# Kernel tuning notes

Measured on AMD Instinct MI355X. Metric: run time of the kernel, lower is better.

## Reference

```python
import jax, jax.numpy as jnp
import numpy as np
import math

# Module constants (from __init__ defaults / chosen init_kwargs)
B = 4            # hand_batch_size
C = 8            # num_cameras
BC = B * C       # camera batch
R = 256          # resolution
NB = 64          # num_bins
BIN = 0.0136     # bin_size
FOV = 33.0       # degrees
DCS = 0.001      # camera_sensor_distance
SIGMA_BIN = 3.0  # self.sigma for soft binning


def _masks():
    fov_rad = FOV * math.pi / 180.0
    scale = math.tan(fov_rad / 2.0)
    center_scale = scale * (1.0 - 1.0 / R)
    lin = jnp.linspace(-center_scale, center_scale, R, dtype=jnp.float32)
    xg, yg = jnp.meshgrid(lin, lin, indexing='xy')
    fm = jnp.stack([xg, -yg, -jnp.ones((R, R), jnp.float32)], axis=2)
    film_mask = -fm / jnp.linalg.norm(fm, axis=2, keepdims=True)  # [R,R,3]
    cos_mask = 1.0 / jnp.sqrt(xg * xg + yg * yg + 1.0)            # [R,R]
    return film_mask, cos_mask


def setup_inputs() -> dict:
    key = jax.random.key(0)
    k1, k2 = jax.random.split(key)
    film_mask, cos_mask = _masks()
    # per-pixel interpolated vertex normals (pre-normalization, as dr.interpolate output)
    normals = jax.random.normal(k1, (BC, R, R, 3), dtype=jnp.float32)
    # per-pixel camera-space intersection points; z ~ 0.5 m so depths fall mid-histogram
    intersections = jax.random.normal(k2, (BC, R, R, 3), dtype=jnp.float32) * 0.1 \
        + jnp.array([0.0, 0.0, 0.5], dtype=jnp.float32)
    return {"normals": normals, "intersections": intersections,
            "film_mask": film_mask, "cos_mask": cos_mask}


def reference(normals, intersections, film_mask, cos_mask):
    width = 2.0 * math.tan(FOV * math.pi / 360.0)
    # cosine foreshortening w.r.t. film ray directions
    dots = jnp.clip(jnp.einsum('ijk,bijk->bij', film_mask, normals), 0.0, 1.0)
    # laser origin offset by 2 * camera_sensor_distance along +x
    laser_points = intersections - jnp.array([2.0 * DCS, 0.0, 0.0], dtype=intersections.dtype)
    laser_distances = jnp.linalg.norm(laser_points, axis=3)  # [BC,R,R]
    laser_tan = jnp.sqrt(laser_points[..., 0] ** 2 + laser_points[..., 1] ** 2) / laser_points[..., 2]
    sig = math.tan(math.radians(21.5)) / 1.4
    laser_mask = jnp.exp(-laser_tan ** 2 / (2.0 * sig * sig))
    dots = dots * laser_mask
    radiance = dots / laser_distances / laser_distances / math.pi \
        * (width * width) * (cos_mask ** 3) / float(R * R)      # [BC,R,R]
    depths = (jnp.linalg.norm(intersections, axis=3) + laser_distances) / 2.0
    d_bin = depths / BIN                                         # [BC,R,R]
    b = jnp.arange(NB, dtype=jnp.float32)                        # [NB]
    # soft bin kernel: sigmoid(s*(d-b)) - sigmoid(s*(d-b-1)), [BC,R,R,NB]
    x = d_bin[..., None] - b
    kernels = jax.nn.sigmoid(SIGMA_BIN * x) - jax.nn.sigmoid(SIGMA_BIN * (x - 1.0))
    # histogram accumulation over all pixels -> per-camera transient [BC,NB]
    transients = jnp.einsum('bijk,bij->bk', kernels, radiance)
    return transients
```

## Files before the change

### kernel.cpp

```cpp
#include <hip/hip_runtime.h>
#include <math.h>

#define NPIX    65536
#define NBINS   64
#define NBATCH  32
#define SPLIT   32
#define BLOCKT  128
#define PXPT    4
#define ITERS   (NPIX / SPLIT / (BLOCKT * PXPT))
#define HSTRIDE 68
#define LDSN    (BLOCKT * HSTRIDE)
#define WIN     12

#define THREE_LOG2E 4.328085122666891f

__global__ __launch_bounds__(BLOCKT, 2) void spad_hist_kernel(
    const float* __restrict__ normals,
    const float* __restrict__ inters,
    const float* __restrict__ film,
    const float* __restrict__ cosm,
    float* __restrict__ ws,
    float kconst, float lmask_c, float half_inv_bin)
{
    __shared__ float hist[LDSN];
    const int tid = threadIdx.x;
    {
        float4* h4 = (float4*)&hist[tid * HSTRIDE];
        #pragma unroll
        for (int i = 0; i < HSTRIDE / 4; ++i) h4[i] = make_float4(0.f, 0.f, 0.f, 0.f);
    }
    __syncthreads();

    const int b = blockIdx.x & (NBATCH - 1);
    const int chunk = blockIdx.x / NBATCH;
    const int pix0 = chunk * (NPIX / SPLIT);
    const int base = tid * HSTRIDE;

    const float E3P[13] = {
        1.0f, 20.085536923187668f, 403.4287934927351f, 8103.083927575384f,
        162754.79141900392f, 3269017.372472111f, 65659969.13733051f,
        1318815734.4832146f, 26489122129.843472f, 532048240601.79865f,
        10686474581524.462f, 214643579785916.06f, 4311231547115195.0f };

    #pragma unroll
    for (int it = 0; it < ITERS; ++it) {
        const int pp = pix0 + (it * BLOCKT + tid) * PXPT;
        const float4* n4 = (const float4*)(normals + ((size_t)b * NPIX + pp) * 3);
        const float4* i4 = (const float4*)(inters  + ((size_t)b * NPIX + pp) * 3);
        const float4* f4 = (const float4*)(film + (size_t)pp * 3);
        const float4  c4 = *(const float4*)(cosm + pp);
        float4 n0 = n4[0], n1 = n4[1], n2 = n4[2];
        float4 i0 = i4[0], i1 = i4[1], i2 = i4[2];
        float4 f0 = f4[0], f1 = f4[1], f2 = f4[2];

        float NX[4] = {n0.x, n0.w, n1.z, n2.y}, NY[4] = {n0.y, n1.x, n1.w, n2.z},
              NZ[4] = {n0.z, n1.y, n2.x, n2.w};
        float IX[4] = {i0.x, i0.w, i1.z, i2.y}, IY[4] = {i0.y, i1.x, i1.w, i2.z},
              IZ[4] = {i0.z, i1.y, i2.x, i2.w};
        float FX[4] = {f0.x, f0.w, f1.z, f2.y}, FY[4] = {f0.y, f1.x, f1.w, f2.z},
              FZ[4] = {f0.z, f1.y, f2.x, f2.w};
        float CM[4] = {c4.x, c4.y, c4.z, c4.w};

        int   K0[4];
        float W[4][WIN];

        #pragma unroll
        for (int p = 0; p < 4; ++p) {
            float dt = FX[p] * NX[p] + FY[p] * NY[p] + FZ[p] * NZ[p];
            dt = fminf(fmaxf(dt, 0.0f), 1.0f);
            float lx = IX[p] - 0.002f;
            float lxy2 = lx * lx + IY[p] * IY[p];
            float l2 = lxy2 + IZ[p] * IZ[p];
            float ld = __builtin_amdgcn_sqrtf(l2);
            float lm = __builtin_amdgcn_exp2f(
                lmask_c * lxy2 * __builtin_amdgcn_rcpf(IZ[p] * IZ[p]));
            float cm3 = CM[p] * CM[p] * CM[p];
            float r = dt * lm * kconst * cm3 * __builtin_amdgcn_rcpf(l2);
            float di = __builtin_amdgcn_sqrtf(
                IX[p] * IX[p] + IY[p] * IY[p] + IZ[p] * IZ[p]);
            float d = (di + ld) * half_inv_bin;

            int j0 = (int)floorf(d);
            j0 = j0 < 4 ? 4 : (j0 > 56 ? 56 : j0);
            int k0 = (j0 - 4) & ~3;
            K0[p] = k0;
            float e0 = __builtin_amdgcn_exp2f(((float)k0 - d) * THREE_LOG2E);
            float S[WIN + 1];
            #pragma unroll
            for (int m = 0; m < WIN + 1; ++m)
                S[m] = __builtin_amdgcn_rcpf(fmaf(e0, E3P[m], 1.0f));
            #pragma unroll
            for (int m = 0; m < WIN; ++m)
                W[p][m] = r * (S[m] - S[m + 1]);
        }

        #pragma unroll
        for (int p = 0; p < 4; ++p) {
            float4* hp = (float4*)&hist[base + K0[p]];
            float4 a = hp[0], bb = hp[1], c = hp[2];
            a.x  += W[p][0];  a.y  += W[p][1];  a.z  += W[p][2];  a.w  += W[p][3];
            bb.x += W[p][4];  bb.y += W[p][5];  bb.z += W[p][6];  bb.w += W[p][7];
            c.x  += W[p][8];  c.y  += W[p][9];  c.z  += W[p][10]; c.w  += W[p][11];
            hp[0] = a; hp[1] = bb; hp[2] = c;
        }
    }
    __syncthreads();

    const int g = tid & 15;
    const int h = tid >> 4;
    float4 acc = make_float4(0.f, 0.f, 0.f, 0.f);
    #pragma unroll
    for (int j = 0; j < 16; ++j) {
        float4 v = *(const float4*)&hist[(h + 8 * j) * HSTRIDE + 4 * g];
        acc.x += v.x; acc.y += v.y; acc.z += v.z; acc.w += v.w;
    }
    __syncthreads();
    *(float4*)&hist[tid * 4] = acc;
    __syncthreads();
    if (tid < 16) {
        float4 s4 = make_float4(0.f, 0.f, 0.f, 0.f);
        #pragma unroll
        for (int hh = 0; hh < 8; ++hh) {
            float4 v = *(const float4*)&hist[hh * 64 + tid * 4];
            s4.x += v.x; s4.y += v.y; s4.z += v.z; s4.w += v.w;
        }
        *(float4*)&ws[(size_t)blockIdx.x * NBINS + tid * 4] = s4;
    }
}

__global__ __launch_bounds__(256) void spad_reduce_kernel(
    const float* __restrict__ ws, float* __restrict__ out)
{
    const int o = blockIdx.x * 256 + threadIdx.x;
    const int b = o >> 6;
    const int k = o & 63;
    float s = 0.0f;
    #pragma unroll
    for (int c = 0; c < SPLIT; ++c)
        s += ws[((size_t)(c * NBATCH + b)) * NBINS + k];
    out[o] = s;
}

extern "C" void kernel_launch(void* const* d_in, const int* in_sizes, int n_in,
                              void* d_out, int out_size, void* d_ws, size_t ws_size,
                              hipStream_t stream) {
    const float* normals = (const float*)d_in[0];
    const float* inters  = (const float*)d_in[1];
    const float* film    = (const float*)d_in[2];
    const float* cosm    = (const float*)d_in[3];
    float* out = (float*)d_out;
    float* ws  = (float*)d_ws;

    const double fov_rad = 33.0 * M_PI / 180.0;
    const double width = 2.0 * tan(fov_rad / 2.0);
    const double kconst_d = width * width / M_PI / 65536.0;
    const double sig = tan(21.5 * M_PI / 180.0) / 1.4;
    const double log2e = 1.4426950408889634;
    const double lmask_c_d = -log2e / (2.0 * sig * sig);
    const double half_inv_bin_d = 0.5 / 0.0136;

    spad_hist_kernel<<<NBATCH * SPLIT, BLOCKT, 0, stream>>>(
        normals, inters, film, cosm, ws,
        (float)kconst_d, (float)lmask_c_d, (float)half_inv_bin_d);

    spad_reduce_kernel<<<(NBATCH * NBINS) / 256, 256, 0, stream>>>(ws, out);
}
```

Before: 92.72 us.

## Share LDS histograms across 16 threads with atomic adds and larger blocks

Each thread previously owned a private 64-bin histogram in LDS, which limited block size and occupancy. Now 16 threads share one histogram and accumulate the 12-bin window with LDS atomicAdd. The window starts exactly at j0-5 instead of a 4-aligned offset. The block grows to 256 threads with 4 blocks per CU, and the final reduction is simplified. In exchange, 12 scalar LDS atomics per pixel replace three float4 read-modify-writes, and threads sharing a histogram can contend on the same bins.

```diff
diff --git a/kernel.cpp b/kernel.cpp
--- a/kernel.cpp
+++ b/kernel.cpp
@@ -5,16 +5,17 @@
 #define NBINS   64
 #define NBATCH  32
 #define SPLIT   32
-#define BLOCKT  128
+#define BLOCKT  256
 #define PXPT    4
 #define ITERS   (NPIX / SPLIT / (BLOCKT * PXPT))
-#define HSTRIDE 68
-#define LDSN    (BLOCKT * HSTRIDE)
 #define WIN     12
+#define NHIST   (BLOCKT / 16)
+#define HSTRIDE 72
+#define LDSN    (NHIST * HSTRIDE)
 
 #define THREE_LOG2E 4.328085122666891f
 
-__global__ __launch_bounds__(BLOCKT, 2) void spad_hist_kernel(
+__global__ __launch_bounds__(BLOCKT, 4) void spad_hist_kernel(
     const float* __restrict__ normals,
     const float* __restrict__ inters,
     const float* __restrict__ film,
@@ -24,17 +25,13 @@
 {
     __shared__ float hist[LDSN];
     const int tid = threadIdx.x;
-    {
-        float4* h4 = (float4*)&hist[tid * HSTRIDE];
-        #pragma unroll
-        for (int i = 0; i < HSTRIDE / 4; ++i) h4[i] = make_float4(0.f, 0.f, 0.f, 0.f);
-    }
+    for (int i = tid; i < LDSN; i += BLOCKT) hist[i] = 0.0f;
     __syncthreads();
 
     const int b = blockIdx.x & (NBATCH - 1);
     const int chunk = blockIdx.x / NBATCH;
     const int pix0 = chunk * (NPIX / SPLIT);
-    const int base = tid * HSTRIDE;
+    float* const hq = &hist[(tid >> 4) * HSTRIDE];
 
     const float E3P[13] = {
         1.0f, 20.085536923187668f, 403.4287934927351f, 8103.083927575384f,
@@ -61,9 +58,6 @@
               FZ[4] = {f0.z, f1.y, f2.x, f2.w};
         float CM[4] = {c4.x, c4.y, c4.z, c4.w};
 
-        int   K0[4];
-        float W[4][WIN];
-
         #pragma unroll
         for (int p = 0; p < 4; ++p) {
             float dt = FX[p] * NX[p] + FY[p] * NY[p] + FZ[p] * NZ[p];
@@ -81,50 +75,27 @@
             float d = (di + ld) * half_inv_bin;
 
             int j0 = (int)floorf(d);
-            j0 = j0 < 4 ? 4 : (j0 > 56 ? 56 : j0);
-            int k0 = (j0 - 4) & ~3;
-            K0[p] = k0;
+            j0 = j0 < 5 ? 5 : (j0 > 57 ? 57 : j0);
+            const int k0 = j0 - 5;
             float e0 = __builtin_amdgcn_exp2f(((float)k0 - d) * THREE_LOG2E);
             float S[WIN + 1];
             #pragma unroll
             for (int m = 0; m < WIN + 1; ++m)
                 S[m] = __builtin_amdgcn_rcpf(fmaf(e0, E3P[m], 1.0f));
+
+            float* hp = hq + k0;
             #pragma unroll
             for (int m = 0; m < WIN; ++m)
-                W[p][m] = r * (S[m] - S[m + 1]);
-        }
-
-        #pragma unroll
-        for (int p = 0; p < 4; ++p) {
-            float4* hp = (float4*)&hist[base + K0[p]];
-            float4 a = hp[0], bb = hp[1], c = hp[2];
-            a.x  += W[p][0];  a.y  += W[p][1];  a.z  += W[p][2];  a.w  += W[p][3];
-            bb.x += W[p][4];  bb.y += W[p][5];  bb.z += W[p][6];  bb.w += W[p][7];
-            c.x  += W[p][8];  c.y  += W[p][9];  c.z  += W[p][10]; c.w  += W[p][11];
-            hp[0] = a; hp[1] = bb; hp[2] = c;
+                atomicAdd(&hp[m], r * (S[m] - S[m + 1]));
         }
     }
     __syncthreads();
 
-    const int g = tid & 15;
-    const int h = tid >> 4;
-    float4 acc = make_float4(0.f, 0.f, 0.f, 0.f);
-    #pragma unroll
-    for (int j = 0; j < 16; ++j) {
-        float4 v = *(const float4*)&hist[(h + 8 * j) * HSTRIDE + 4 * g];
-        acc.x += v.x; acc.y += v.y; acc.z += v.z; acc.w += v.w;
-    }
-    __syncthreads();
-    *(float4*)&hist[tid * 4] = acc;
-    __syncthreads();
-    if (tid < 16) {
-        float4 s4 = make_float4(0.f, 0.f, 0.f, 0.f);
+    if (tid < NBINS) {
+        float s = 0.0f;
         #pragma unroll
-        for (int hh = 0; hh < 8; ++hh) {
-            float4 v = *(const float4*)&hist[hh * 64 + tid * 4];
-            s4.x += v.x; s4.y += v.y; s4.z += v.z; s4.w += v.w;
-        }
-        *(float4*)&ws[(size_t)blockIdx.x * NBINS + tid * 4] = s4;
+        for (int h = 0; h < NHIST; ++h) s += hist[h * HSTRIDE + tid];
+        ws[(size_t)blockIdx.x * NBINS + tid] = s;
     }
 }
 
```

New measurement: 207.9 us. 124% more time.
